# Kernel tuning notes

Measured on AMD Instinct MI355X. Metric: run time of the kernel, lower is better.

## Reference

```python
import jax, jax.numpy as jnp
import numpy as np

BN_EPS = 1e-5
L2_EPS = 1e-12


def batch_norm(x, gamma, beta):
    # training-mode BN over the node (batch) dimension, matching nn.BatchNorm1d forward
    mu = x.mean(axis=0)
    var = x.var(axis=0)
    return gamma * (x - mu) * jax.lax.rsqrt(var + BN_EPS) + beta


def sage_gcn(x, src, dst, W, b):
    # DGL SAGEConv(aggregator_type='gcn'): h = (sum_{u->v} x_u + x_v) / (deg_in(v) + 1); out = h @ W + b
    n = x.shape[0]
    deg = jax.ops.segment_sum(jnp.ones(src.shape, x.dtype), dst, num_segments=n)
    neigh = jax.ops.segment_sum(x[src], dst, num_segments=n)  # [N, d] gather + scatter-add
    h = (neigh + x) / (deg[:, None] + 1.0)
    return h @ W + b


def setup_inputs() -> dict:
    key = jax.random.key(0)
    ks = jax.random.split(key, 32)
    N, E = 50000, 800000
    IN, HID, NC = 128, 128, 64
    inp = {}
    inp['x'] = jax.random.normal(ks[0], (N, IN), jnp.float32)
    for i, g in enumerate(['1', '2', '3']):
        inp['src' + g] = jax.random.randint(ks[1 + 2 * i], (E,), 0, N, jnp.int32)
        inp['dst' + g] = jax.random.randint(ks[2 + 2 * i], (E,), 0, N, jnp.int32)
    def lin(k, din, dout):
        k1, k2 = jax.random.split(k)
        s = 1.0 / np.sqrt(din)
        return (jax.random.uniform(k1, (din, dout), jnp.float32, -s, s),
                jax.random.uniform(k2, (dout,), jnp.float32, -s, s))
    inp['W11'], inp['b11'] = lin(ks[8], IN, HID)
    inp['W21'], inp['b21'] = lin(ks[9], IN, HID)
    inp['W31'], inp['b31'] = lin(ks[10], IN, HID)
    inp['W12'], inp['b12'] = lin(ks[11], HID, NC)
    inp['W22'], inp['b22'] = lin(ks[12], HID, NC)
    inp['W32'], inp['b32'] = lin(ks[13], HID, NC)
    inp['g1'] = jnp.ones((IN,), jnp.float32); inp['be1'] = jnp.zeros((IN,), jnp.float32)
    inp['g2'] = jnp.ones((HID,), jnp.float32); inp['be2'] = jnp.zeros((HID,), jnp.float32)
    inp['g3'] = jnp.ones((NC,), jnp.float32); inp['be3'] = jnp.zeros((NC,), jnp.float32)
    return inp


def reference(x, src1, dst1, src2, dst2, src3, dst3,
              W11, b11, W21, b21, W31, b31,
              W12, b12, W22, b22, W32, b32,
              g1, be1, g2, be2, g3, be3):
    x = batch_norm(x, g1, be1)  # dropout omitted (identity) for determinism
    h = (sage_gcn(x, src1, dst1, W11, b11)
         + sage_gcn(x, src2, dst2, W21, b21)
         + sage_gcn(x, src3, dst3, W31, b31))
    h = jax.nn.relu(h)
    h = batch_norm(h, g2, be2)
    z = (sage_gcn(h, src1, dst1, W12, b12)
         + sage_gcn(h, src2, dst2, W22, b22)
         + sage_gcn(h, src3, dst3, W32, b32))
    z = batch_norm(z, g3, be3)
    z = jax.nn.sigmoid(z)
    # per-row min-max scale
    zmax = z.max(axis=1, keepdims=True)
    zmin = z.min(axis=1, keepdims=True)
    z = (z - zmin) / (zmax - zmin)
    # F.normalize (row L2, eps=1e-12)
    norm = jnp.maximum(jnp.linalg.norm(z, axis=1, keepdims=True), L2_EPS)
    return z / norm
```

## Files before the change

kernel.cpp:

```cpp
#include <hip/hip_runtime.h>
#include <math.h>

constexpr int FDIM = 128;
constexpr int ODIM = 64;
constexpr int BINB = 512;
constexpr int NBK  = 256;
constexpr int CSB  = 512;

typedef short bf16x8 __attribute__((ext_vector_type(8)));
typedef float f32x4  __attribute__((ext_vector_type(4)));

__device__ inline unsigned short f2bf(float f) {
    unsigned u = __float_as_uint(f);
    u = (u + 0x7fffu + ((u >> 16) & 1u)) >> 16;
    return (unsigned short)u;
}
__device__ inline float bf2f(unsigned short s) { return __uint_as_float(((unsigned)s) << 16); }
__device__ inline float blo(unsigned v) { return __uint_as_float(v << 16); }
__device__ inline float bhi(unsigned v) { return __uint_as_float(v & 0xffff0000u); }

__global__ __launch_bounds__(256) void k_cs128(const float* __restrict__ X, int N,
                                               float* __restrict__ partial,
                                               unsigned short* __restrict__ XB) {
    const int t = threadIdx.x;
    const int rh = t >> 7, c = t & 127;
    const int rows_per = (N + gridDim.x - 1) / gridDim.x;
    const int r0 = blockIdx.x * rows_per;
    const int r1 = min(N, r0 + rows_per);
    float s = 0.f, ss = 0.f;
    for (int r = r0 + rh; r < r1; r += 2) {
        const float v = X[(size_t)r * 128 + c];
        s += v;
        ss += v * v;
        XB[(size_t)r * 128 + c] = f2bf(v);
    }
    __shared__ float shs[256], shss[256];
    shs[t] = s;
    shss[t] = ss;
    __syncthreads();
    if (rh == 0) {
        partial[(size_t)blockIdx.x * 256 + c]       = s + shs[t + 128];
        partial[(size_t)blockIdx.x * 256 + 128 + c] = ss + shss[t + 128];
    }
}

__global__ __launch_bounds__(256) void k_cs64(const float* __restrict__ X, int N,
                                              float* __restrict__ partial) {
    const int t = threadIdx.x;
    const int rh = t >> 6, c = t & 63;
    const int rows_per = (N + gridDim.x - 1) / gridDim.x;
    const int r0 = blockIdx.x * rows_per;
    const int r1 = min(N, r0 + rows_per);
    float s = 0.f, ss = 0.f;
    for (int r = r0 + rh; r < r1; r += 4) {
        const float v = X[(size_t)r * 64 + c];
        s += v;
        ss += v * v;
    }
    __shared__ float shs[256], shss[256];
    shs[t] = s;
    shss[t] = ss;
    __syncthreads();
    if (rh == 0) {
        partial[(size_t)blockIdx.x * 128 + c] =
            s + shs[t + 64] + shs[t + 128] + shs[t + 192];
        partial[(size_t)blockIdx.x * 128 + 64 + c] =
            ss + shss[t + 64] + shss[t + 128] + shss[t + 192];
    }
}

template<int C>
__global__ __launch_bounds__(256) void k_fin(const float* __restrict__ partial, int nb, int N,
                                             const float* __restrict__ gamma,
                                             const float* __restrict__ beta,
                                             float* __restrict__ scale,
                                             float* __restrict__ shift) {
    const int c = blockIdx.x;
    const int t = threadIdx.x;
    float s = 0.f, ss = 0.f;
    for (int b = t; b < nb; b += 256) {
        s  += partial[(size_t)b * (2 * C) + c];
        ss += partial[(size_t)b * (2 * C) + C + c];
    }
    __shared__ float shs[256], shss[256];
    shs[t] = s;
    shss[t] = ss;
    __syncthreads();
    for (int o = 128; o; o >>= 1) {
        if (t < o) { shs[t] += shs[t + o]; shss[t] += shss[t + o]; }
        __syncthreads();
    }
    if (t == 0) {
        const float mu  = shs[0] / (float)N;
        const float var = shss[0] / (float)N - mu * mu;
        const float sc  = gamma[c] * rsqrtf(var + 1e-5f);
        scale[c] = sc;
        shift[c] = beta[c] - mu * sc;
    }
}

__global__ void k_wt(const float* __restrict__ W1, const float* __restrict__ W2,
                     const float* __restrict__ W3, unsigned short* __restrict__ WTb) {
    const int g = blockIdx.y;
    const float* W = (g == 0) ? W1 : (g == 1) ? W2 : W3;
    const int id = blockIdx.x * 256 + threadIdx.x;
    const int n = id >> 7, k = id & 127;
    WTb[(size_t)g * 16384 + (size_t)n * 128 + k] = f2bf(W[(size_t)k * 128 + n]);
}

__global__ void k_wt2(const float* __restrict__ s2,
                      const float* __restrict__ W1, const float* __restrict__ W2,
                      const float* __restrict__ W3, unsigned short* __restrict__ W2Tb) {
    const int g = blockIdx.y;
    const float* W = (g == 0) ? W1 : (g == 1) ? W2 : W3;
    const int id = blockIdx.x * 256 + threadIdx.x;
    const int n = id >> 7, k = id & 127;
    W2Tb[(size_t)g * 8192 + (size_t)n * 128 + k] = f2bf(s2[k] * W[(size_t)k * ODIM + n]);
}

__global__ __launch_bounds__(256) void k_c2(const float* __restrict__ sh2,
                                            const float* __restrict__ W1,
                                            const float* __restrict__ W2,
                                            const float* __restrict__ W3,
                                            float* __restrict__ c2) {
    const int g = blockIdx.x;
    const int t = threadIdx.x;
    const int n = t & 63, kq = t >> 6;
    const float* W = (g == 0) ? W1 : (g == 1) ? W2 : W3;
    float s = 0.f;
    for (int k = kq * 32; k < kq * 32 + 32; ++k)
        s = fmaf(sh2[k], W[(size_t)k * ODIM + n], s);
    __shared__ float red[256];
    red[t] = s;
    __syncthreads();
    if (kq == 0) c2[g * ODIM + n] = red[n] + red[64 + n] + red[128 + n] + red[192 + n];
}

__global__ __launch_bounds__(256) void k_bincount(
    const int* __restrict__ d0, const int* __restrict__ d1, const int* __restrict__ d2,
    int e0, int e1, int e2, unsigned* __restrict__ cnts) {
    const int g = blockIdx.y, blk = blockIdx.x, t = threadIdx.x;
    const int* dst = (g == 0) ? d0 : (g == 1) ? d1 : d2;
    const int E = (g == 0) ? e0 : (g == 1) ? e1 : e2;
    __shared__ unsigned hist[NBK];
    hist[t] = 0;
    __syncthreads();
    const int chunk = (E + BINB - 1) / BINB;
    const int i0 = blk * chunk, i1 = min(E, i0 + chunk);
    for (int i = i0 + t; i < i1; i += 256) atomicAdd(&hist[((unsigned)dst[i]) >> 8], 1u);
    __syncthreads();
    cnts[((size_t)(g * NBK + t)) * BINB + blk] = hist[t];
}

__global__ __launch_bounds__(256) void k_sa(const unsigned* __restrict__ cnts,
                                            unsigned* __restrict__ bs) {
    const int blk = blockIdx.x, t = threadIdx.x;
    unsigned s = cnts[(size_t)blk * 512 + t] + cnts[(size_t)blk * 512 + 256 + t];
    __shared__ unsigned red[256];
    red[t] = s;
    __syncthreads();
    for (int o = 128; o; o >>= 1) {
        if (t < o) red[t] += red[t + o];
        __syncthreads();
    }
    if (t == 0) bs[blk] = red[0];
}

__global__ void k_sb(unsigned* __restrict__ bs, int n) {
    const int t = threadIdx.x;
    __shared__ unsigned ps[1024];
    unsigned v = (t < n) ? bs[t] : 0u;
    ps[t] = v;
    __syncthreads();
    for (int o = 1; o < 1024; o <<= 1) {
        const unsigned a = (t >= o) ? ps[t - o] : 0u;
        __syncthreads();
        ps[t] += a;
        __syncthreads();
    }
    if (t < n) bs[t] = ps[t] - v;
}

__global__ __launch_bounds__(256) void k_sc(unsigned* __restrict__ cnts,
                                            const unsigned* __restrict__ bs) {
    const int blk = blockIdx.x, t = threadIdx.x;
    const size_t base = (size_t)blk * 512;
    const unsigned e0v = cnts[base + 2 * t];
    const unsigned e1v = cnts[base + 2 * t + 1];
    const unsigned pair = e0v + e1v;
    __shared__ unsigned ps[256];
    ps[t] = pair;
    __syncthreads();
    for (int o = 1; o < 256; o <<= 1) {
        const unsigned a = (t >= o) ? ps[t - o] : 0u;
        __syncthreads();
        ps[t] += a;
        __syncthreads();
    }
    const unsigned ex = ps[t] - pair + bs[blk];
    cnts[base + 2 * t]     = ex;
    cnts[base + 2 * t + 1] = ex + e0v;
}

__global__ __launch_bounds__(256) void k_binplace(
    const int* __restrict__ s0, const int* __restrict__ d0,
    const int* __restrict__ s1, const int* __restrict__ d1,
    const int* __restrict__ s2, const int* __restrict__ d2,
    int e0, int e1, int e2, const unsigned* __restrict__ pos, unsigned* __restrict__ ebuf) {
    const int g = blockIdx.y, blk = blockIdx.x, t = threadIdx.x;
    const int* src = (g == 0) ? s0 : (g == 1) ? s1 : s2;
    const int* dst = (g == 0) ? d0 : (g == 1) ? d1 : d2;
    const int E = (g == 0) ? e0 : (g == 1) ? e1 : e2;
    __shared__ unsigned cur[NBK];
    cur[t] = pos[((size_t)(g * NBK + t)) * BINB + blk];
    __syncthreads();
    const int chunk = (E + BINB - 1) / BINB;
    const int i0 = blk * chunk, i1 = min(E, i0 + chunk);
    for (int i = i0 + t; i < i1; i += 256) {
        const unsigned dv = (unsigned)dst[i];
        const unsigned p = atomicAdd(&cur[dv >> 8], 1u);
        ebuf[p] = (unsigned)src[i] | ((dv & 255u) << 16);
    }
}

__global__ __launch_bounds__(256) void k_build(
    const unsigned* __restrict__ ebuf, const unsigned* __restrict__ pos,
    int etot, int e0, int e1,
    int* __restrict__ off, int* __restrict__ cend, float* __restrict__ rinv,
    int* __restrict__ n0, int* __restrict__ n1, int* __restrict__ n2, int N) {
    const int g = blockIdx.y, b = blockIdx.x, t = threadIdx.x;
    const int v0 = b << 8;
    const int gbase = (g == 0) ? 0 : ((g == 1) ? e0 : e0 + e1);
    int* nbr = (g == 0) ? n0 : ((g == 1) ? n1 : n2);
    const int cell = g * NBK + b;
    const unsigned seg0 = pos[(size_t)cell * BINB];
    const unsigned seg1 = (cell + 1 < 3 * NBK) ? pos[(size_t)(cell + 1) * BINB] : (unsigned)etot;

    __shared__ unsigned deg[NBK];
    __shared__ unsigned ps[NBK];
    __shared__ unsigned cur[NBK];
    deg[t] = 0;
    __syncthreads();
    for (unsigned i = seg0 + t; i < seg1; i += 256)
        atomicAdd(&deg[(ebuf[i] >> 16) & 255u], 1u);
    __syncthreads();
    const unsigned dv = deg[t];
    ps[t] = dv;
    __syncthreads();
    for (int o = 1; o < 256; o <<= 1) {
        const unsigned a = (t >= o) ? ps[t - o] : 0u;
        __syncthreads();
        ps[t] += a;
        __syncthreads();
    }
    const unsigned ex = ps[t] - dv;
    const int nbase = (int)seg0 - gbase;
    const int node = v0 + t;
    if (node < N) {
        off[(size_t)g * N + node]  = nbase + (int)ex;
        cend[(size_t)g * N + node] = nbase + (int)(ex + dv);
        rinv[(size_t)g * N + node] = 1.0f / ((float)dv + 1.0f);
    }
    cur[t] = ex;
    __syncthreads();
    for (unsigned i = seg0 + t; i < seg1; i += 256) {
        const unsigned e = ebuf[i];
        const unsigned p = atomicAdd(&cur[(e >> 16) & 255u], 1u);
        nbr[nbase + (int)p] = (int)(e & 0xFFFFu);
    }
}

__global__ __launch_bounds__(256) void k_gather3(
    const unsigned short* __restrict__ XB,
    const int* __restrict__ nbr0, const int* __restrict__ nbr1, const int* __restrict__ nbr2,
    const int* __restrict__ off, const int* __restrict__ cend,
    const float* __restrict__ rinv, const float* __restrict__ s1,
    const float* __restrict__ sh1, unsigned short* __restrict__ AGG3b, int N) {
    const int g = blockIdx.y;
    const int* nbr = (g == 0) ? nbr0 : (g == 1) ? nbr1 : nbr2;
    const int gb = g * N;
    const int wave = threadIdx.x >> 6;
    const int lane = threadIdx.x & 63;
    const int v = blockIdx.x * 4 + wave;
    if (v >= N) return;
    const int i0 = off[gb + v], i1 = cend[gb + v];
    const int l2 = lane * 2;
    unsigned sv = ((const unsigned*)(XB + (size_t)v * FDIM))[lane];
    float2 acc;
    acc.x = blo(sv);
    acc.y = bhi(sv);
    int i = i0;
    for (; i + 8 <= i1; i += 8) {
        const int u0 = nbr[i],     u1 = nbr[i + 1], u2 = nbr[i + 2], u3 = nbr[i + 3];
        const int u4 = nbr[i + 4], u5 = nbr[i + 5], u6 = nbr[i + 6], u7 = nbr[i + 7];
        const unsigned a0 = ((const unsigned*)(XB + (size_t)u0 * FDIM))[lane];
        const unsigned a1 = ((const unsigned*)(XB + (size_t)u1 * FDIM))[lane];
        const unsigned a2 = ((const unsigned*)(XB + (size_t)u2 * FDIM))[lane];
        const unsigned a3 = ((const unsigned*)(XB + (size_t)u3 * FDIM))[lane];
        const unsigned a4 = ((const unsigned*)(XB + (size_t)u4 * FDIM))[lane];
        const unsigned a5 = ((const unsigned*)(XB + (size_t)u5 * FDIM))[lane];
        const unsigned a6 = ((const unsigned*)(XB + (size_t)u6 * FDIM))[lane];
        const unsigned a7 = ((const unsigned*)(XB + (size_t)u7 * FDIM))[lane];
        acc.x += ((blo(a0) + blo(a1)) + (blo(a2) + blo(a3))) + ((blo(a4) + blo(a5)) + (blo(a6) + blo(a7)));
        acc.y += ((bhi(a0) + bhi(a1)) + (bhi(a2) + bhi(a3))) + ((bhi(a4) + bhi(a5)) + (bhi(a6) + bhi(a7)));
    }
    for (; i < i1; ++i) {
        const unsigned a = ((const unsigned*)(XB + (size_t)nbr[i] * FDIM))[lane];
        acc.x += blo(a);
        acc.y += bhi(a);
    }
    const float r = rinv[gb + v];
    const float2 sc = *(const float2*)&s1[l2];
    const float2 sh = *(const float2*)&sh1[l2];
    const float ox = fmaf(acc.x * r, sc.x, sh.x);
    const float oy = fmaf(acc.y * r, sc.y, sh.y);
    const unsigned w = (unsigned)f2bf(ox) | ((unsigned)f2bf(oy) << 16);
    ((unsigned*)(AGG3b + ((size_t)(gb + v)) * FDIM))[lane] = w;
}

__global__ __launch_bounds__(256) void k_gemm1(
    const unsigned short* __restrict__ AGG3b, const unsigned short* __restrict__ WTb,
    const float* __restrict__ b1, const float* __restrict__ b2, const float* __restrict__ b3,
    unsigned short* __restrict__ Hb, float* __restrict__ partial, int N) {
    constexpr int AST = 40;
    __shared__ __align__(16) unsigned short As[64 * AST];
    __shared__ __align__(16) unsigned short Bs[128 * AST];
    __shared__ float sst[4][128], ssq[4][128];
    const int t = threadIdx.x;
    const int w = t >> 6, l = t & 63;
    const int row0 = blockIdx.x * 64;
    const int cl = l & 15;
    const int hi = l >> 4;
    f32x4 acc[8] = {};

    for (int g = 0; g < 3; ++g) {
        const unsigned short* Ag = AGG3b + (size_t)g * N * FDIM;
        const unsigned short* Wg = WTb + (size_t)g * 16384;
        for (int kb = 0; kb < 4; ++kb) {
            const int k0 = kb * 32;
            {
                const int r = t >> 2, h = t & 3;
                const int row = row0 + r;
                uint4 v = make_uint4(0u, 0u, 0u, 0u);
                if (row < N) v = *(const uint4*)(Ag + (size_t)row * FDIM + k0 + h * 8);
                *(uint4*)(As + r * AST + h * 8) = v;
            }
            {
                const int c = t >> 1, p = t & 1;
                const uint4 v0 = *(const uint4*)(Wg + (size_t)c * 128 + k0 + p * 16);
                const uint4 v1 = *(const uint4*)(Wg + (size_t)c * 128 + k0 + p * 16 + 8);
                *(uint4*)(Bs + c * AST + p * 16)     = v0;
                *(uint4*)(Bs + c * AST + p * 16 + 8) = v1;
            }
            __syncthreads();
            const bf16x8 af = *(const bf16x8*)(As + (w * 16 + cl) * AST + hi * 8);
            #pragma unroll
            for (int c = 0; c < 8; ++c) {
                const bf16x8 bf = *(const bf16x8*)(Bs + (c * 16 + cl) * AST + hi * 8);
                acc[c] = __builtin_amdgcn_mfma_f32_16x16x32_bf16(af, bf, acc[c], 0, 0, 0);
            }
            __syncthreads();
        }
    }
    float s8[8], q8[8];
    #pragma unroll
    for (int c = 0; c < 8; ++c) {
        const int col = c * 16 + cl;
        const float bb = b1[col] + b2[col] + b3[col];
        float s = 0.f, q = 0.f;
        #pragma unroll
        for (int r = 0; r < 4; ++r) {
            const int row = row0 + w * 16 + hi * 4 + r;
            if (row < N) {
                const unsigned short hb = f2bf(fmaxf(acc[c][r] + bb, 0.f));
                Hb[(size_t)row * FDIM + col] = hb;
                const float h = bf2f(hb);
                s += h;
                q += h * h;
            }
        }
        s8[c] = s;
        q8[c] = q;
    }
    #pragma unroll
    for (int c = 0; c < 8; ++c) {
        s8[c] += __shfl_xor(s8[c], 16, 64); s8[c] += __shfl_xor(s8[c], 32, 64);
        q8[c] += __shfl_xor(q8[c], 16, 64); q8[c] += __shfl_xor(q8[c], 32, 64);
    }
    if (hi == 0) {
        #pragma unroll
        for (int c = 0; c < 8; ++c) {
            sst[w][c * 16 + cl] = s8[c];
            ssq[w][c * 16 + cl] = q8[c];
        }
    }
    __syncthreads();
    if (t < 128) {
        partial[(size_t)blockIdx.x * 256 + t]       = sst[0][t] + sst[1][t] + sst[2][t] + sst[3][t];
        partial[(size_t)blockIdx.x * 256 + 128 + t] = ssq[0][t] + ssq[1][t] + ssq[2][t] + ssq[3][t];
    }
}

__global__ __launch_bounds__(256) void k_gemm2(
    const unsigned short* __restrict__ Hb, const unsigned short* __restrict__ W2Tb,
    const float* __restrict__ c2, unsigned short* __restrict__ Ub, int N) {
    constexpr int AST = 40;
    __shared__ __align__(16) unsigned short As[64 * AST];
    __shared__ __align__(16) unsigned short Bs[64 * AST];
    const int t = threadIdx.x;
    const int g = blockIdx.y;
    const int w = t >> 6, l = t & 63;
    const int row0 = blockIdx.x * 64;
    const int cl = l & 15;
    const int hi = l >> 4;
    const unsigned short* Wg = W2Tb + (size_t)g * 8192;
    f32x4 acc[4] = {};

    for (int kb = 0; kb < 4; ++kb) {
        const int k0 = kb * 32;
        {
            const int r = t >> 2, h = t & 3;
            const int row = row0 + r;
            uint4 v = make_uint4(0u, 0u, 0u, 0u);
            if (row < N) v = *(const uint4*)(Hb + (size_t)row * FDIM + k0 + h * 8);
            *(uint4*)(As + r * AST + h * 8) = v;
        }
        {
            const int c = t >> 2, h = t & 3;
            const uint4 v = *(const uint4*)(Wg + (size_t)c * 128 + k0 + h * 8);
            *(uint4*)(Bs + c * AST + h * 8) = v;
        }
        __syncthreads();
        const bf16x8 af = *(const bf16x8*)(As + (w * 16 + cl) * AST + hi * 8);
        #pragma unroll
        for (int c = 0; c < 4; ++c) {
            const bf16x8 bf = *(const bf16x8*)(Bs + (c * 16 + cl) * AST + hi * 8);
            acc[c] = __builtin_amdgcn_mfma_f32_16x16x32_bf16(af, bf, acc[c], 0, 0, 0);
        }
        __syncthreads();
    }
    const float* cg = c2 + (size_t)g * ODIM;
    unsigned short* Ug = Ub + (size_t)g * N * ODIM;
    #pragma unroll
    for (int c = 0; c < 4; ++c) {
        const int col = c * 16 + cl;
        const float bb = cg[col];
        #pragma unroll
        for (int r = 0; r < 4; ++r) {
            const int row = row0 + w * 16 + hi * 4 + r;
            if (row < N) Ug[(size_t)row * ODIM + col] = f2bf(acc[c][r] + bb);
        }
    }
}

__global__ __launch_bounds__(256) void k_gc64(
    const unsigned short* __restrict__ Ub,
    const int* __restrict__ nbr0, const int* __restrict__ nbr1, const int* __restrict__ nbr2,
    const int* __restrict__ off, const int* __restrict__ cend,
    const float* __restrict__ rinv,
    const float* __restrict__ b1, const float* __restrict__ b2, const float* __restrict__ b3,
    float* __restrict__ Z, int N) {
    const int wave = threadIdx.x >> 6;
    const int lane = threadIdx.x & 63;
    const int v = blockIdx.x * 4 + wave;
    if (v >= N) return;
    const size_t gs = (size_t)N * ODIM;
    float z = b1[lane] + b2[lane] + b3[lane];
    #pragma unroll
    for (int g = 0; g < 3; ++g) {
        const unsigned short* Ug = Ub + (size_t)g * gs;
        const int* nb = (g == 0) ? nbr0 : (g == 1) ? nbr1 : nbr2;
        const int i0 = off[g * N + v], i1 = cend[g * N + v];
        float s = bf2f(Ug[(size_t)v * ODIM + lane]);
        int i = i0;
        for (; i + 8 <= i1; i += 8) {
            const int u0 = nb[i],     u1 = nb[i + 1], u2 = nb[i + 2], u3 = nb[i + 3];
            const int u4 = nb[i + 4], u5 = nb[i + 5], u6 = nb[i + 6], u7 = nb[i + 7];
            const float a0 = bf2f(Ug[(size_t)u0 * ODIM + lane]);
            const float a1 = bf2f(Ug[(size_t)u1 * ODIM + lane]);
            const float a2 = bf2f(Ug[(size_t)u2 * ODIM + lane]);
            const float a3 = bf2f(Ug[(size_t)u3 * ODIM + lane]);
            const float a4 = bf2f(Ug[(size_t)u4 * ODIM + lane]);
            const float a5 = bf2f(Ug[(size_t)u5 * ODIM + lane]);
            const float a6 = bf2f(Ug[(size_t)u6 * ODIM + lane]);
            const float a7 = bf2f(Ug[(size_t)u7 * ODIM + lane]);
            s += ((a0 + a1) + (a2 + a3)) + ((a4 + a5) + (a6 + a7));
        }
        for (; i < i1; ++i) s += bf2f(Ug[(size_t)nb[i] * ODIM + lane]);
        z += s * rinv[g * N + v];
    }
    Z[(size_t)v * ODIM + lane] = z;
}

__global__ __launch_bounds__(256) void k_final(float* __restrict__ Z,
                                               const float* __restrict__ scale,
                                               const float* __restrict__ shift, int N) {
    const int wave = threadIdx.x >> 6;
    const int lane = threadIdx.x & 63;
    const int row = blockIdx.x * 4 + wave;
    if (row >= N) return;
    float v = fmaf(Z[(size_t)row * ODIM + lane], scale[lane], shift[lane]);
    float s = 1.0f / (1.0f + expf(-v));
    float mn = s, mx = s;
    #pragma unroll
    for (int off = 32; off; off >>= 1) {
        mn = fminf(mn, __shfl_xor(mn, off, 64));
        mx = fmaxf(mx, __shfl_xor(mx, off, 64));
    }
    const float sc = (s - mn) / (mx - mn);
    float sq = sc * sc;
    #pragma unroll
    for (int off = 32; off; off >>= 1) sq += __shfl_xor(sq, off, 64);
    const float norm = fmaxf(sqrtf(sq), 1e-12f);
    Z[(size_t)row * ODIM + lane] = sc / norm;
}

extern "C" void kernel_launch(void* const* d_in, const int* in_sizes, int n_in,
                              void* d_out, int out_size, void* d_ws, size_t ws_size,
                              hipStream_t stream) {
    const float* x = (const float*)d_in[0];
    const int* src[3] = {(const int*)d_in[1], (const int*)d_in[3], (const int*)d_in[5]};
    const int* dst[3] = {(const int*)d_in[2], (const int*)d_in[4], (const int*)d_in[6]};
    const int E[3] = {in_sizes[1], in_sizes[3], in_sizes[5]};
    const int Etot = E[0] + E[1] + E[2];
    const float* W11 = (const float*)d_in[7];  const float* b11 = (const float*)d_in[8];
    const float* W21 = (const float*)d_in[9];  const float* b21 = (const float*)d_in[10];
    const float* W31 = (const float*)d_in[11]; const float* b31 = (const float*)d_in[12];
    const float* W12 = (const float*)d_in[13]; const float* b12 = (const float*)d_in[14];
    const float* W22 = (const float*)d_in[15]; const float* b22 = (const float*)d_in[16];
    const float* W32 = (const float*)d_in[17]; const float* b32 = (const float*)d_in[18];
    const float* g1  = (const float*)d_in[19]; const float* be1 = (const float*)d_in[20];
    const float* g2  = (const float*)d_in[21]; const float* be2 = (const float*)d_in[22];
    const float* g3  = (const float*)d_in[23]; const float* be3 = (const float*)d_in[24];
    const int N = in_sizes[0] / FDIM;
    float* Z = (float*)d_out;
    const int gblocks1 = (N + 63) / 64;

    float* ws   = (float*)d_ws;
    float* Hreg = ws;
    unsigned short* xb = (unsigned short*)Hreg;
    unsigned short* Hb = (unsigned short*)Hreg;
    float* REG  = Hreg + (size_t)N * FDIM;
    unsigned short* AGG3b = (unsigned short*)REG;
    unsigned short* Ub = (unsigned short*)REG;
    unsigned* ebuf = (unsigned*)REG;
    unsigned* cnts = ebuf + (size_t)Etot;
    unsigned* bs   = cnts + (size_t)3 * NBK * BINB;
    float* rinv = REG + (size_t)3 * N * FDIM;
    float* partial = rinv + (size_t)3 * N;
    const size_t psz = (size_t)((gblocks1 > CSB ? gblocks1 : CSB)) * 256;
    float* s1  = partial + psz;    float* sh1 = s1 + 128;
    float* s2  = sh1 + 128;        float* sh2 = s2 + 128;
    float* s3  = sh2 + 128;        float* sh3 = s3 + 64;
    float* c2  = sh3 + 64;
    unsigned short* WTb  = (unsigned short*)(c2 + 3 * ODIM);
    unsigned short* W2Tb = WTb + (size_t)3 * 16384;
    int* off  = (int*)(W2Tb + (size_t)3 * 8192);
    int* cend = off + (size_t)3 * N;
    int* nbr  = cend + (size_t)3 * N;
    int* nbrg[3];
    nbrg[0] = nbr;
    nbrg[1] = nbrg[0] + E[0];
    nbrg[2] = nbrg[1] + E[1];

    const int nbuckets = (N + 255) >> 8;
    k_bincount<<<dim3(BINB, 3), 256, 0, stream>>>(dst[0], dst[1], dst[2],
                                                  E[0], E[1], E[2], cnts);
    k_sa<<<3 * NBK * BINB / 512, 256, 0, stream>>>(cnts, bs);
    k_sb<<<1, 1024, 0, stream>>>(bs, 3 * NBK * BINB / 512);
    k_sc<<<3 * NBK * BINB / 512, 256, 0, stream>>>(cnts, bs);
    k_binplace<<<dim3(BINB, 3), 256, 0, stream>>>(src[0], dst[0], src[1], dst[1],
                                                  src[2], dst[2], E[0], E[1], E[2],
                                                  cnts, ebuf);
    k_build<<<dim3(nbuckets, 3), 256, 0, stream>>>(ebuf, cnts, Etot, E[0], E[1],
                                                   off, cend, rinv,
                                                   nbrg[0], nbrg[1], nbrg[2], N);

    k_cs128<<<CSB, 256, 0, stream>>>(x, N, partial, xb);
    k_fin<128><<<128, 256, 0, stream>>>(partial, CSB, N, g1, be1, s1, sh1);
    k_wt<<<dim3(64, 3), 256, 0, stream>>>(W11, W21, W31, WTb);

    const int gblocks = (N + 3) / 4;
    k_gather3<<<dim3(gblocks, 3), 256, 0, stream>>>(xb, nbrg[0], nbrg[1], nbrg[2],
                                                    off, cend, rinv, s1, sh1, AGG3b, N);
    k_gemm1<<<gblocks1, 256, 0, stream>>>(AGG3b, WTb, b11, b21, b31, Hb, partial, N);

    k_fin<128><<<128, 256, 0, stream>>>(partial, gblocks1, N, g2, be2, s2, sh2);
    k_c2<<<3, 256, 0, stream>>>(sh2, W12, W22, W32, c2);
    k_wt2<<<dim3(32, 3), 256, 0, stream>>>(s2, W12, W22, W32, W2Tb);

    dim3 grid2(gblocks1, 3);
    k_gemm2<<<grid2, 256, 0, stream>>>(Hb, W2Tb, c2, Ub, N);
    k_gc64<<<gblocks, 256, 0, stream>>>(Ub, nbrg[0], nbrg[1], nbrg[2], off, cend, rinv,
                                        b12, b22, b32, Z, N);

    k_cs64<<<CSB, 256, 0, stream>>>(Z, N, partial);
    k_fin<64><<<64, 256, 0, stream>>>(partial, CSB, N, g3, be3, s3, sh3);
    k_final<<<(N + 3) / 4, 256, 0, stream>>>(Z, s3, sh3, N);
}
```

Before: 352.4 us.

## Split first-layer gather into four feature-quarter passes for cache locality

The first-layer neighbour gather is split into four launches, each covering one 64-byte quarter of the 128-wide bf16 feature row. Each 16-lane group handles one node, so a block processes 16 nodes per launch. The aim is to shrink each pass's random-access working set (50000 rows × 64 B) so it fits in L2/MALL, which should cut miss traffic on the random gathers. In exchange, the neighbour index lists are read four times, each random gather fetches only 64 B, and there are extra launches.

```diff
diff --git a/kernel.cpp b/kernel.cpp
--- a/kernel.cpp
+++ b/kernel.cpp
@@ -270,52 +270,52 @@
     }
 }
 
-__global__ __launch_bounds__(256) void k_gather3(
+__global__ __launch_bounds__(256) void k_gather3q(
     const unsigned short* __restrict__ XB,
     const int* __restrict__ nbr0, const int* __restrict__ nbr1, const int* __restrict__ nbr2,
     const int* __restrict__ off, const int* __restrict__ cend,
     const float* __restrict__ rinv, const float* __restrict__ s1,
-    const float* __restrict__ sh1, unsigned short* __restrict__ AGG3b, int N) {
+    const float* __restrict__ sh1, unsigned short* __restrict__ AGG3b, int N, int q) {
     const int g = blockIdx.y;
     const int* nbr = (g == 0) ? nbr0 : (g == 1) ? nbr1 : nbr2;
     const int gb = g * N;
-    const int wave = threadIdx.x >> 6;
-    const int lane = threadIdx.x & 63;
-    const int v = blockIdx.x * 4 + wave;
+    const int t = threadIdx.x;
+    const int grp = t >> 4;
+    const int l16 = t & 15;
+    const int v = blockIdx.x * 16 + grp;
     if (v >= N) return;
     const int i0 = off[gb + v], i1 = cend[gb + v];
-    const int l2 = lane * 2;
-    unsigned sv = ((const unsigned*)(XB + (size_t)v * FDIM))[lane];
-    float2 acc;
-    acc.x = blo(sv);
-    acc.y = bhi(sv);
+    const int cu = q * 16 + l16;
+    const unsigned* Xu = (const unsigned*)XB;
+    const unsigned sv = Xu[(size_t)v * 64 + cu];
+    float ax = blo(sv), ay = bhi(sv);
     int i = i0;
     for (; i + 8 <= i1; i += 8) {
         const int u0 = nbr[i],     u1 = nbr[i + 1], u2 = nbr[i + 2], u3 = nbr[i + 3];
         const int u4 = nbr[i + 4], u5 = nbr[i + 5], u6 = nbr[i + 6], u7 = nbr[i + 7];
-        const unsigned a0 = ((const unsigned*)(XB + (size_t)u0 * FDIM))[lane];
-        const unsigned a1 = ((const unsigned*)(XB + (size_t)u1 * FDIM))[lane];
-        const unsigned a2 = ((const unsigned*)(XB + (size_t)u2 * FDIM))[lane];
-        const unsigned a3 = ((const unsigned*)(XB + (size_t)u3 * FDIM))[lane];
-        const unsigned a4 = ((const unsigned*)(XB + (size_t)u4 * FDIM))[lane];
-        const unsigned a5 = ((const unsigned*)(XB + (size_t)u5 * FDIM))[lane];
-        const unsigned a6 = ((const unsigned*)(XB + (size_t)u6 * FDIM))[lane];
-        const unsigned a7 = ((const unsigned*)(XB + (size_t)u7 * FDIM))[lane];
-        acc.x += ((blo(a0) + blo(a1)) + (blo(a2) + blo(a3))) + ((blo(a4) + blo(a5)) + (blo(a6) + blo(a7)));
-        acc.y += ((bhi(a0) + bhi(a1)) + (bhi(a2) + bhi(a3))) + ((bhi(a4) + bhi(a5)) + (bhi(a6) + bhi(a7)));
+        const unsigned a0 = Xu[(size_t)u0 * 64 + cu];
+        const unsigned a1 = Xu[(size_t)u1 * 64 + cu];
+        const unsigned a2 = Xu[(size_t)u2 * 64 + cu];
+        const unsigned a3 = Xu[(size_t)u3 * 64 + cu];
+        const unsigned a4 = Xu[(size_t)u4 * 64 + cu];
+        const unsigned a5 = Xu[(size_t)u5 * 64 + cu];
+        const unsigned a6 = Xu[(size_t)u6 * 64 + cu];
+        const unsigned a7 = Xu[(size_t)u7 * 64 + cu];
+        ax += ((blo(a0) + blo(a1)) + (blo(a2) + blo(a3))) + ((blo(a4) + blo(a5)) + (blo(a6) + blo(a7)));
+        ay += ((bhi(a0) + bhi(a1)) + (bhi(a2) + bhi(a3))) + ((bhi(a4) + bhi(a5)) + (bhi(a6) + bhi(a7)));
     }
     for (; i < i1; ++i) {
-        const unsigned a = ((const unsigned*)(XB + (size_t)nbr[i] * FDIM))[lane];
-        acc.x += blo(a);
-        acc.y += bhi(a);
+        const unsigned a = Xu[(size_t)nbr[i] * 64 + cu];
+        ax += blo(a);
+        ay += bhi(a);
     }
     const float r = rinv[gb + v];
-    const float2 sc = *(const float2*)&s1[l2];
-    const float2 sh = *(const float2*)&sh1[l2];
-    const float ox = fmaf(acc.x * r, sc.x, sh.x);
-    const float oy = fmaf(acc.y * r, sc.y, sh.y);
-    const unsigned w = (unsigned)f2bf(ox) | ((unsigned)f2bf(oy) << 16);
-    ((unsigned*)(AGG3b + ((size_t)(gb + v)) * FDIM))[lane] = w;
+    const float2 sc = *(const float2*)&s1[cu * 2];
+    const float2 sh = *(const float2*)&sh1[cu * 2];
+    const float ox = fmaf(ax * r, sc.x, sh.x);
+    const float oy = fmaf(ay * r, sc.y, sh.y);
+    ((unsigned*)AGG3b)[((size_t)(gb + v)) * 64 + cu] =
+        (unsigned)f2bf(ox) | ((unsigned)f2bf(oy) << 16);
 }
 
 __global__ __launch_bounds__(256) void k_gemm1(
@@ -580,9 +580,11 @@
     k_fin<128><<<128, 256, 0, stream>>>(partial, CSB, N, g1, be1, s1, sh1);
     k_wt<<<dim3(64, 3), 256, 0, stream>>>(W11, W21, W31, WTb);
 
-    const int gblocks = (N + 3) / 4;
-    k_gather3<<<dim3(gblocks, 3), 256, 0, stream>>>(xb, nbrg[0], nbrg[1], nbrg[2],
-                                                    off, cend, rinv, s1, sh1, AGG3b, N);
+    const int qblocks = (N + 15) / 16;
+    for (int q = 0; q < 4; ++q)
+        k_gather3q<<<dim3(qblocks, 3), 256, 0, stream>>>(xb, nbrg[0], nbrg[1], nbrg[2],
+                                                         off, cend, rinv, s1, sh1,
+                                                         AGG3b, N, q);
     k_gemm1<<<gblocks1, 256, 0, stream>>>(AGG3b, WTb, b11, b21, b31, Hb, partial, N);
 
     k_fin<128><<<128, 256, 0, stream>>>(partial, gblocks1, N, g2, be2, s2, sh2);
@@ -591,6 +593,7 @@
 
     dim3 grid2(gblocks1, 3);
     k_gemm2<<<grid2, 256, 0, stream>>>(Hb, W2Tb, c2, Ub, N);
+    const int gblocks = (N + 3) / 4;
     k_gc64<<<gblocks, 256, 0, stream>>>(Ub, nbrg[0], nbrg[1], nbrg[2], off, cend, rinv,
                                         b12, b22, b32, Z, N);
 
```

After: 406.5 us. 1.15x slower.
